# Performance work log

Measured on AMD Instinct MI355X. Metric: run time of the kernel, lower is better.

Reference implementation:

```python
import jax, jax.numpy as jnp
import numpy as np

V, D, H, L, B, T = 32000, 1024, 16, 4, 2, 2048
DH = D // H
F = 4 * D
EPS = 1e-5


def setup_inputs() -> dict:
    key = jax.random.key(0)
    ks = jax.random.split(key, 16)
    s = 0.02
    n = lambda k, shape: (jax.random.normal(k, shape, jnp.float32) * s)
    inp = {
        "idx": jax.random.randint(ks[0], (B, T), 0, V, dtype=jnp.int64),
        "tok_emb": n(ks[1], (V, D)),
        "pos_emb": n(ks[2], (1, T, D)),
        # per-layer stacked params; Linear weights stored as (in, out)
        "Wq": n(ks[3], (L, D, D)), "bq": jnp.zeros((L, D)),
        "Wk": n(ks[4], (L, D, D)), "bk": jnp.zeros((L, D)),
        "Wv": n(ks[5], (L, D, D)), "bv": jnp.zeros((L, D)),
        "Wo": n(ks[6], (L, D, D)), "bo": jnp.zeros((L, D)),
        "ln1_g": jnp.ones((L, D)), "ln1_b": jnp.zeros((L, D)),
        "W1": n(ks[7], (L, D, F)), "b1": jnp.zeros((L, F)),
        "W2": n(ks[8], (L, F, D)), "b2": jnp.zeros((L, D)),
        "ln2_g": jnp.ones((L, D)), "ln2_b": jnp.zeros((L, D)),
        "lnf_g": jnp.ones((D,)), "lnf_b": jnp.zeros((D,)),
        "lm_W": n(ks[9], (D, V)),
    }
    return inp


def _ln(x, g, b):
    m = jnp.mean(x, axis=-1, keepdims=True)
    v = jnp.mean(jnp.square(x - m), axis=-1, keepdims=True)
    return (x - m) * jax.lax.rsqrt(v + EPS) * g + b


def _band_attn(x, Wq, bq, Wk, bk, Wv, bv, Wo, bo):
    # width-3 causal band: query t attends to keys {t, t-1, t-2}
    b_, t_, _ = x.shape
    q = (x @ Wq + bq).reshape(b_, t_, H, DH)
    k = (x @ Wk + bk).reshape(b_, t_, H, DH)
    v = (x @ Wv + bv).reshape(b_, t_, H, DH)

    def shift(a, o):  # align key at position t-o with query t
        return jnp.pad(a, ((0, 0), (o, 0), (0, 0), (0, 0)))[:, :t_]

    ks_ = jnp.stack([shift(k, o) for o in range(3)], axis=-2)  # (B,T,H,3,DH)
    vs_ = jnp.stack([shift(v, o) for o in range(3)], axis=-2)
    scale = 1.0 / np.sqrt(DH)
    scores = jnp.einsum('bthd,bthod->btho', q, ks_) * scale       # (B,T,H,3)
    pos = jnp.arange(t_)[None, :, None, None]
    off = jnp.arange(3)[None, None, None, :]
    scores = jnp.where(pos >= off, scores, -jnp.inf)
    p = jax.nn.softmax(scores, axis=-1)
    y = jnp.einsum('btho,bthod->bthd', p, vs_).reshape(b_, t_, D)
    return y @ Wo + bo


def reference(idx, tok_emb, pos_emb, Wq, bq, Wk, bk, Wv, bv, Wo, bo,
              ln1_g, ln1_b, W1, b1, W2, b2, ln2_g, ln2_b, lnf_g, lnf_b, lm_W):
    t_ = idx.shape[1]
    x = tok_emb[idx] + pos_emb[:, :t_, :]
    for i in range(L):
        h = _ln(x, ln1_g[i], ln1_b[i])
        x = x + _band_attn(h, Wq[i], bq[i], Wk[i], bk[i], Wv[i], bv[i], Wo[i], bo[i])
        h = _ln(x, ln2_g[i], ln2_b[i])
        h = jax.nn.gelu(h @ W1[i] + b1[i], approximate=False) @ W2[i] + b2[i]
        x = x + h
    x = _ln(x, lnf_g, lnf_b)
    logits = x @ lm_W
    return logits
```

## Files before the change

### kernel.cpp

```cpp
#include <hip/hip_runtime.h>
#include <cstdint>
#include <cstddef>

#define MROWS   4096
#define TSEQ    2048
#define DMODEL  1024
#define NHEAD   16
#define FFN     4096
#define NVOCAB  32000
#define NLAYER  4

typedef float  f32x4  __attribute__((ext_vector_type(4)));
typedef __bf16 bf16x8 __attribute__((ext_vector_type(8)));

#define VMCNT(n) asm volatile("s_waitcnt vmcnt(" #n ")" ::: "memory")
#define LGKM0()  asm volatile("s_waitcnt lgkmcnt(0)" ::: "memory")

__device__ __forceinline__ unsigned short f2bf(float f) {
    unsigned u = __builtin_bit_cast(unsigned, f);
    u += 0x7fffu + ((u >> 16) & 1u);
    return (unsigned short)(u >> 16);
}
__device__ __forceinline__ float bf2f(unsigned short u) {
    return __builtin_bit_cast(float, (unsigned)u << 16);
}

__device__ __forceinline__ float gelu_exact(float v) {
    return 0.5f * v * (1.0f + erff(v * 0.7071067811865476f));
}

__global__ __launch_bounds__(256) void embed_kernel(const int* __restrict__ idx,
                                                    const float* __restrict__ tok,
                                                    const float* __restrict__ pos,
                                                    float* __restrict__ x) {
    int row = blockIdx.x, tid = threadIdx.x;
    int token = idx[row];
    int t = row & (TSEQ - 1);
    float4 a = ((const float4*)(tok + (size_t)token * DMODEL))[tid];
    float4 p = ((const float4*)(pos + (size_t)t * DMODEL))[tid];
    a.x += p.x; a.y += p.y; a.z += p.z; a.w += p.w;
    ((float4*)(x + (size_t)row * DMODEL))[tid] = a;
}

__global__ __launch_bounds__(256) void ln_kernel(const float* __restrict__ x,
                                                 const float* __restrict__ g,
                                                 const float* __restrict__ b,
                                                 unsigned short* __restrict__ out) {
    int row = blockIdx.x, tid = threadIdx.x;
    float4 v = ((const float4*)(x + (size_t)row * DMODEL))[tid];
    float s1 = v.x + v.y + v.z + v.w;
    float s2 = v.x * v.x + v.y * v.y + v.z * v.z + v.w * v.w;
    for (int s = 32; s; s >>= 1) { s1 += __shfl_xor(s1, s); s2 += __shfl_xor(s2, s); }
    __shared__ float red[8];
    int lane = tid & 63, w = tid >> 6;
    if (lane == 0) { red[w] = s1; red[4 + w] = s2; }
    __syncthreads();
    s1 = red[0] + red[1] + red[2] + red[3];
    s2 = red[4] + red[5] + red[6] + red[7];
    float mean = s1 * (1.0f / DMODEL);
    float var  = s2 * (1.0f / DMODEL) - mean * mean;
    float rs   = rsqrtf(var + 1e-5f);
    float4 gv = ((const float4*)g)[tid];
    float4 bv = ((const float4*)b)[tid];
    size_t o = (size_t)row * DMODEL + tid * 4;
    out[o + 0] = f2bf((v.x - mean) * rs * gv.x + bv.x);
    out[o + 1] = f2bf((v.y - mean) * rs * gv.y + bv.y);
    out[o + 2] = f2bf((v.z - mean) * rs * gv.z + bv.z);
    out[o + 3] = f2bf((v.w - mean) * rs * gv.w + bv.w);
}

__global__ __launch_bounds__(256) void transpose_bf16(const float* __restrict__ W,
                                                      unsigned short* __restrict__ WT,
                                                      int K, int ldW) {
    __shared__ float tile[64][65];
    int n0 = blockIdx.x * 64, k0 = blockIdx.y * 64;
    int tid = threadIdx.x;
    int lr4 = tid & 15;
    int rw  = tid >> 4;
#pragma unroll
    for (int p = 0; p < 4; ++p) {
        int k = rw + p * 16;
        float4 v = *(const float4*)(W + (size_t)(k0 + k) * ldW + n0 + lr4 * 4);
        tile[k][lr4 * 4 + 0] = v.x;
        tile[k][lr4 * 4 + 1] = v.y;
        tile[k][lr4 * 4 + 2] = v.z;
        tile[k][lr4 * 4 + 3] = v.w;
    }
    __syncthreads();
    int kc = tid & 15;
    int nr = tid >> 4;
#pragma unroll
    for (int p = 0; p < 4; ++p) {
        int n = nr + p * 16;
        ushort4 o;
        o.x = f2bf(tile[kc * 4 + 0][n]);
        o.y = f2bf(tile[kc * 4 + 1][n]);
        o.z = f2bf(tile[kc * 4 + 2][n]);
        o.w = f2bf(tile[kc * 4 + 3][n]);
        *(ushort4*)(WT + (size_t)(n0 + n) * K + k0 + kc * 4) = o;
    }
}

__global__ __launch_bounds__(256) void transpose_qkv(const float* __restrict__ Wq,
                                                     const float* __restrict__ Wk,
                                                     const float* __restrict__ Wv,
                                                     unsigned short* __restrict__ WT) {
    __shared__ float tile[64][65];
    const float* W = (blockIdx.z == 0) ? Wq : (blockIdx.z == 1) ? Wk : Wv;
    unsigned short* dst = WT + (size_t)blockIdx.z * DMODEL * DMODEL;
    int n0 = blockIdx.x * 64, k0 = blockIdx.y * 64;
    int tid = threadIdx.x;
    int lr4 = tid & 15, rw = tid >> 4;
#pragma unroll
    for (int p = 0; p < 4; ++p) {
        int k = rw + p * 16;
        float4 v = *(const float4*)(W + (size_t)(k0 + k) * DMODEL + n0 + lr4 * 4);
        tile[k][lr4 * 4 + 0] = v.x;
        tile[k][lr4 * 4 + 1] = v.y;
        tile[k][lr4 * 4 + 2] = v.z;
        tile[k][lr4 * 4 + 3] = v.w;
    }
    __syncthreads();
    int kc = tid & 15, nr = tid >> 4;
#pragma unroll
    for (int p = 0; p < 4; ++p) {
        int n = nr + p * 16;
        ushort4 o;
        o.x = f2bf(tile[kc * 4 + 0][n]);
        o.y = f2bf(tile[kc * 4 + 1][n]);
        o.z = f2bf(tile[kc * 4 + 2][n]);
        o.w = f2bf(tile[kc * 4 + 3][n]);
        *(ushort4*)(dst + (size_t)(n0 + n) * DMODEL + k0 + kc * 4) = o;
    }
}

__global__ __launch_bounds__(256) void pack_qkv_bias(const float* __restrict__ bq,
                                                     const float* __restrict__ bk,
                                                     const float* __restrict__ bv,
                                                     float* __restrict__ dst) {
    int i = blockIdx.x * 256 + threadIdx.x;
    int l = i / 3072, c = i % 3072;
    float v = (c < 1024) ? bq[l * 1024 + c]
            : (c < 2048) ? bk[l * 1024 + c - 1024]
                         : bv[l * 1024 + c - 2048];
    dst[i] = v;
}

__global__ __launch_bounds__(256) void combine2(const float* __restrict__ p0,
                                                const float* __restrict__ p1,
                                                const float* __restrict__ bias,
                                                float* __restrict__ x) {
    int i = blockIdx.x * 256 + threadIdx.x;
    float4 a = ((const float4*)p0)[i];
    float4 b = ((const float4*)p1)[i];
    float4 xv = ((float4*)x)[i];
    int col = (i * 4) & (DMODEL - 1);
    float4 bb = *(const float4*)(bias + col);
    xv.x += a.x + b.x + bb.x;
    xv.y += a.y + b.y + bb.y;
    xv.z += a.z + b.z + bb.z;
    xv.w += a.w + b.w + bb.w;
    ((float4*)x)[i] = xv;
}

__global__ __launch_bounds__(256) void attn_kernel(const unsigned short* __restrict__ qkv,
                                                   unsigned short* __restrict__ y) {
    int wid  = (blockIdx.x * 256 + threadIdx.x) >> 6;
    int lane = threadIdx.x & 63;
    int h = wid & (NHEAD - 1);
    int row = wid >> 4;
    int t = row & (TSEQ - 1);
    const unsigned short* base = qkv + (size_t)row * 3072 + h * 64;
    float qd = bf2f(base[lane]);
    float d0 = qd * bf2f(base[1024 + lane]);
    float d1 = (t >= 1) ? qd * bf2f(base[1024 - 3072 + lane]) : 0.0f;
    float d2 = (t >= 2) ? qd * bf2f(base[1024 - 6144 + lane]) : 0.0f;
    for (int s = 32; s; s >>= 1) {
        d0 += __shfl_xor(d0, s); d1 += __shfl_xor(d1, s); d2 += __shfl_xor(d2, s);
    }
    d0 *= 0.125f; d1 *= 0.125f; d2 *= 0.125f;
    float m = d0;
    if (t >= 1) m = fmaxf(m, d1);
    if (t >= 2) m = fmaxf(m, d2);
    float p0 = expf(d0 - m);
    float p1 = (t >= 1) ? expf(d1 - m) : 0.0f;
    float p2 = (t >= 2) ? expf(d2 - m) : 0.0f;
    float den = p0 + p1 + p2;
    float v0 = bf2f(base[2048 + lane]);
    float v1 = (t >= 1) ? bf2f(base[2048 - 3072 + lane]) : 0.0f;
    float v2 = (t >= 2) ? bf2f(base[2048 - 6144 + lane]) : 0.0f;
    float yv = (p0 * v0 + p1 * v1 + p2 * v2) / den;
    y[(size_t)row * DMODEL + h * 64 + lane] = f2bf(yv);
}

template <int EPI>
__global__ __launch_bounds__(256, 3) void gemmv2(const unsigned short* __restrict__ A,
                                                 const unsigned short* __restrict__ BT,
                                                 const float* __restrict__ bias,
                                                 const float* __restrict__ res,
                                                 float* __restrict__ outF,
                                                 unsigned short* __restrict__ outB,
                                                 int M, int N, int Ks, int KL, int ldc) {
    __shared__ unsigned short As[2][4096];
    __shared__ unsigned short Bs[2][4096];
    const int tid = threadIdx.x;
    const int lane = tid & 63, wid = tid >> 6;
    const int wr = wid >> 1, wc = wid & 1;
    const int lr = lane & 15, kq = lane >> 4;

    const int nbm = M >> 7;
    const int nwg = gridDim.x;
    int orig = blockIdx.x;
    int q8 = nwg >> 3, r8 = nwg & 7;
    int xcd = orig & 7, lin = orig >> 3;
    int wg = (xcd < r8 ? xcd * (q8 + 1) : r8 * (q8 + 1) + (xcd - r8) * q8) + lin;
    int bm = wg % nbm, bn = wg / nbm;
    const int kc = blockIdx.y;

    const unsigned short* Ab = A + (size_t)bm * 128 * Ks + (size_t)kc * KL;
    const unsigned short* Bb = BT + (size_t)bn * 128 * Ks + (size_t)kc * KL;

    int sOff[2];
#pragma unroll
    for (int i = 0; i < 2; ++i) {
        int pc = i * 256 + tid;
        int line = pc >> 3, slot = pc & 7;
        int row = line * 2 + (slot >> 2);
        int c = (slot & 3) ^ (line & 3);
        sOff[i] = row * Ks + c * 8;
    }

#define STAGEV2(T) do {                                                                        \
    unsigned short* dA_ = &As[(T) & 1][0];                                                     \
    unsigned short* dB_ = &Bs[(T) & 1][0];                                                     \
    _Pragma("unroll") for (int i_ = 0; i_ < 2; ++i_) {                                         \
        __builtin_amdgcn_global_load_lds(                                                      \
            (const __attribute__((address_space(1))) void*)(Ab + sOff[i_] + (T) * 32),         \
            (__attribute__((address_space(3))) void*)(dA_ + (size_t)(i_ * 256 + tid) * 8), 16, 0, 0); \
        __builtin_amdgcn_global_load_lds(                                                      \
            (const __attribute__((address_space(1))) void*)(Bb + sOff[i_] + (T) * 32),         \
            (__attribute__((address_space(3))) void*)(dB_ + (size_t)(i_ * 256 + tid) * 8), 16, 0, 0); \
    }                                                                                          \
} while (0)

    const int slot = ((lane & 1) << 2) | (kq ^ ((lr >> 1) & 3));
    const int laneOff = ((lr >> 1) << 6) + slot * 8;
    int aOff[4], bOff[4];
#pragma unroll
    for (int m = 0; m < 4; ++m) aOff[m] = wr * 2048 + m * 512 + laneOff;
#pragma unroll
    for (int n = 0; n < 4; ++n) bOff[n] = wc * 2048 + n * 512 + laneOff;

    f32x4 acc[4][4] = {};
    const int nt = KL >> 5;

    STAGEV2(0);
    __syncthreads();

    for (int t = 0; t < nt; ++t) {
        const bool pf = (t + 1) < nt;
        if (pf) STAGEV2(t + 1);
        const unsigned short* sA = &As[t & 1][0];
        const unsigned short* sB = &Bs[t & 1][0];
        bf16x8 a[4], b[4];
#pragma unroll
        for (int m = 0; m < 4; ++m) a[m] = *(const bf16x8*)(sA + aOff[m]);
#pragma unroll
        for (int n = 0; n < 4; ++n) b[n] = *(const bf16x8*)(sB + bOff[n]);
        __builtin_amdgcn_s_setprio(1);
#pragma unroll
        for (int m = 0; m < 4; ++m)
#pragma unroll
            for (int n = 0; n < 4; ++n)
                acc[m][n] = __builtin_amdgcn_mfma_f32_16x16x32_bf16(a[m], b[n], acc[m][n], 0, 0, 0);
        __builtin_amdgcn_s_setprio(0);
        if (pf) __syncthreads();
    }

    const int row0 = bm * 128 + wr * 64;
    const int col0 = bn * 128 + wc * 64;
    float* outP = (EPI == 0) ? (outF + (size_t)kc * M * ldc) : outF;
#pragma unroll
    for (int m = 0; m < 4; ++m) {
#pragma unroll
        for (int n = 0; n < 4; ++n) {
            int col = col0 + n * 16 + lr;
            int rbase = row0 + m * 16 + kq * 4;
            float bb = (EPI != 0 && bias) ? bias[col] : 0.0f;
#pragma unroll
            for (int j = 0; j < 4; ++j) {
                size_t off = (size_t)(rbase + j) * ldc + col;
                float v = acc[m][n][j] + bb;
                if (EPI == 1) v += res[off];
                if (EPI == 2)      outB[off] = f2bf(gelu_exact(v));
                else               outP[off] = v;
            }
        }
    }
#undef STAGEV2
}

template <int EPI>
__global__ __launch_bounds__(512, 2) void gemm256(const unsigned short* __restrict__ A,
                                                  const unsigned short* __restrict__ BT,
                                                  const float* __restrict__ bias,
                                                  const float* __restrict__ res,
                                                  float* __restrict__ outF,
                                                  unsigned short* __restrict__ outB,
                                                  int M, int N, int K, int ldc) {
    __shared__ unsigned short As[2][2][8192];
    __shared__ unsigned short Bs[2][2][8192];
    const int tid = threadIdx.x;
    const int lane = tid & 63, wid = tid >> 6;
    const int wr = wid >> 2, wc = wid & 3;
    const int lr = lane & 15, kq = lane >> 4;

    const int nbm = M >> 8;
    const int nwg = gridDim.x;
    int orig = blockIdx.x;
    int q8 = nwg >> 3, r8 = nwg & 7;
    int xcd = orig & 7, lin = orig >> 3;
    int wg = (xcd < r8 ? xcd * (q8 + 1) : r8 * (q8 + 1) + (xcd - r8) * q8) + lin;
    int bm = wg % nbm, bn = wg / nbm;

    const unsigned short* Ab = A + (size_t)bm * 256 * K;
    const unsigned short* Bb = BT + (size_t)bn * 256 * K;

    int sG0, sG1;
    {
        int pc0 = tid,        l0 = pc0 >> 3, s0 = pc0 & 7;
        int pc1 = 512 + tid,  l1 = pc1 >> 3, s1 = pc1 & 7;
        sG0 = (l0 * 2 + (s0 >> 2)) * K + (((s0 & 3) ^ (l0 & 3)) * 8);
        sG1 = (l1 * 2 + (s1 >> 2)) * K + (((s1 & 3) ^ (l1 & 3)) * 8);
    }

#define STAGE256(REGION, GBASE, TT, KH) do {                                                   \
    __builtin_amdgcn_global_load_lds(                                                          \
        (const __attribute__((address_space(1))) void*)((GBASE) + sG0 + (TT) * 64 + (KH) * 32),\
        (__attribute__((address_space(3))) void*)((REGION) + (size_t)tid * 8), 16, 0, 0);      \
    __builtin_amdgcn_global_load_lds(                                                          \
        (const __attribute__((address_space(1))) void*)((GBASE) + sG1 + (TT) * 64 + (KH) * 32),\
        (__attribute__((address_space(3))) void*)((REGION) + (size_t)(512 + tid) * 8), 16, 0, 0);\
} while (0)

    const int slot = ((lane & 1) << 2) | (kq ^ ((lr >> 1) & 3));
    const int laneOff = ((lr >> 1) << 6) + slot * 8;
    const int aBase = wr * 4096 + laneOff;
    const int bBase = wc * 2048 + laneOff;

    f32x4 acc[8][4] = {};
    const int nt = K >> 6;

    STAGE256(&As[0][0][0], Ab, 0, 0);
    STAGE256(&Bs[0][0][0], Bb, 0, 0);
    STAGE256(&As[0][1][0], Ab, 0, 1);
    STAGE256(&Bs[0][1][0], Bb, 0, 1);
    VMCNT(4);
    __builtin_amdgcn_s_barrier();

    for (int t = 0; t < nt; ++t) {
        const int buf = t & 1;
        const bool pf = (t + 1) < nt;
        const unsigned short* A0 = &As[buf][0][0];
        const unsigned short* A1 = &As[buf][1][0];
        const unsigned short* B0 = &Bs[buf][0][0];
        const unsigned short* B1 = &Bs[buf][1][0];
        unsigned short* nA0 = &As[buf ^ 1][0][0];
        unsigned short* nA1 = &As[buf ^ 1][1][0];
        unsigned short* nB0 = &Bs[buf ^ 1][0][0];
        unsigned short* nB1 = &Bs[buf ^ 1][1][0];

        bf16x8 a[8], b0, b1;

#pragma unroll
        for (int m = 0; m < 8; ++m) a[m] = *(const bf16x8*)(A0 + aBase + m * 512);
        b0 = *(const bf16x8*)(B0 + bBase + 0 * 512);
        b1 = *(const bf16x8*)(B0 + bBase + 1 * 512);
        if (pf) STAGE256(nA0, Ab, t + 1, 0);
        __builtin_amdgcn_s_barrier();
        LGKM0();
        __builtin_amdgcn_s_setprio(1);
#pragma unroll
        for (int m = 0; m < 8; ++m) {
            acc[m][0] = __builtin_amdgcn_mfma_f32_16x16x32_bf16(a[m], b0, acc[m][0], 0, 0, 0);
            acc[m][1] = __builtin_amdgcn_mfma_f32_16x16x32_bf16(a[m], b1, acc[m][1], 0, 0, 0);
        }
        __builtin_amdgcn_s_setprio(0);
        __builtin_amdgcn_s_barrier();

        b0 = *(const bf16x8*)(B0 + bBase + 2 * 512);
        b1 = *(const bf16x8*)(B0 + bBase + 3 * 512);
        if (pf) STAGE256(nB0, Bb, t + 1, 0);
        __builtin_amdgcn_s_barrier();
        LGKM0();
        __builtin_amdgcn_s_setprio(1);
#pragma unroll
        for (int m = 0; m < 8; ++m) {
            acc[m][2] = __builtin_amdgcn_mfma_f32_16x16x32_bf16(a[m], b0, acc[m][2], 0, 0, 0);
            acc[m][3] = __builtin_amdgcn_mfma_f32_16x16x32_bf16(a[m], b1, acc[m][3], 0, 0, 0);
        }
        __builtin_amdgcn_s_setprio(0);
        if (pf) VMCNT(4); else VMCNT(0);
        __builtin_amdgcn_s_barrier();

#pragma unroll
        for (int m = 0; m < 8; ++m) a[m] = *(const bf16x8*)(A1 + aBase + m * 512);
        b0 = *(const bf16x8*)(B1 + bBase + 0 * 512);
        b1 = *(const bf16x8*)(B1 + bBase + 1 * 512);
        if (pf) STAGE256(nA1, Ab, t + 1, 1);
        __builtin_amdgcn_s_barrier();
        LGKM0();
        __builtin_amdgcn_s_setprio(1);
#pragma unroll
        for (int m = 0; m < 8; ++m) {
            acc[m][0] = __builtin_amdgcn_mfma_f32_16x16x32_bf16(a[m], b0, acc[m][0], 0, 0, 0);
            acc[m][1] = __builtin_amdgcn_mfma_f32_16x16x32_bf16(a[m], b1, acc[m][1], 0, 0, 0);
        }
        __builtin_amdgcn_s_setprio(0);
        __builtin_amdgcn_s_barrier();

        b0 = *(const bf16x8*)(B1 + bBase + 2 * 512);
        b1 = *(const bf16x8*)(B1 + bBase + 3 * 512);
        if (pf) STAGE256(nB1, Bb, t + 1, 1);
        __builtin_amdgcn_s_barrier();
        LGKM0();
        __builtin_amdgcn_s_setprio(1);
#pragma unroll
        for (int m = 0; m < 8; ++m) {
            acc[m][2] = __builtin_amdgcn_mfma_f32_16x16x32_bf16(a[m], b0, acc[m][2], 0, 0, 0);
            acc[m][3] = __builtin_amdgcn_mfma_f32_16x16x32_bf16(a[m], b1, acc[m][3], 0, 0, 0);
        }
        __builtin_amdgcn_s_setprio(0);
        if (pf) VMCNT(4);
        __builtin_amdgcn_s_barrier();
    }

    const int row0 = bm * 256 + wr * 128;
    const int col0 = bn * 256 + wc * 64;
#pragma unroll
    for (int m = 0; m < 8; ++m) {
#pragma unroll
        for (int n = 0; n < 4; ++n) {
            int col = col0 + n * 16 + lr;
            int rbase = row0 + m * 16 + kq * 4;
            float bb = bias ? bias[col] : 0.0f;
#pragma unroll
            for (int j = 0; j < 4; ++j) {
                size_t off = (size_t)(rbase + j) * ldc + col;
                float v = acc[m][n][j] + bb;
                if (EPI == 1) v += res[off];
                if (EPI == 2)      outB[off] = f2bf(gelu_exact(v));
                else if (EPI == 3) outB[off] = f2bf(v);
                else               outF[off] = v;
            }
        }
    }
#undef STAGE256
}

extern "C" void kernel_launch(void* const* d_in, const int* in_sizes, int n_in,
                              void* d_out, int out_size, void* d_ws, size_t ws_size,
                              hipStream_t stream) {
    const int*   idx  = (const int*)d_in[0];
    const float* tok  = (const float*)d_in[1];
    const float* pos  = (const float*)d_in[2];
    const float* Wq   = (const float*)d_in[3];
    const float* bq   = (const float*)d_in[4];
    const float* Wk   = (const float*)d_in[5];
    const float* bk   = (const float*)d_in[6];
    const float* Wv   = (const float*)d_in[7];
    const float* bv   = (const float*)d_in[8];
    const float* Wo   = (const float*)d_in[9];
    const float* bo   = (const float*)d_in[10];
    const float* ln1g = (const float*)d_in[11];
    const float* ln1b = (const float*)d_in[12];
    const float* W1   = (const float*)d_in[13];
    const float* b1   = (const float*)d_in[14];
    const float* W2   = (const float*)d_in[15];
    const float* b2   = (const float*)d_in[16];
    const float* ln2g = (const float*)d_in[17];
    const float* ln2b = (const float*)d_in[18];
    const float* lnfg = (const float*)d_in[19];
    const float* lnfb = (const float*)d_in[20];
    const float* lmW  = (const float*)d_in[21];

    const bool bigws = ws_size >= (92ull << 20);

    char* ws = (char*)d_ws;
    unsigned short* wbuf;
    unsigned short* hbuf;
    unsigned short* ybuf;
    unsigned short* xfbuf;
    float*          bqkv;
    if (bigws) {
        wbuf  = (unsigned short*)(ws);
        hbuf  = (unsigned short*)(ws + (63ull << 20));
        ybuf  = (unsigned short*)(ws + (71ull << 20));
        xfbuf = (unsigned short*)(ws + (79ull << 20));
        bqkv  = (float*)(ws + (87ull << 20));
    } else {
        wbuf  = (unsigned short*)(ws);
        hbuf  = (unsigned short*)(ws + (16u << 20));
        ybuf  = (unsigned short*)(ws + (24u << 20));
        xfbuf = (unsigned short*)(ws + (32u << 20));
        bqkv  = (float*)(ws + (40u << 20));
    }

    float* outF = (float*)d_out;
    float* xbuf = outF;
    unsigned short* qkv = (unsigned short*)((char*)d_out + (16ull << 20));
    unsigned short* hidden = (unsigned short*)((char*)d_out + (64ull << 20));
    float* pbuf = (float*)((char*)d_out + (96ull << 20));

    embed_kernel<<<MROWS, 256, 0, stream>>>(idx, tok, pos, xbuf);
    pack_qkv_bias<<<(NLAYER * 3072) / 256, 256, 0, stream>>>(bq, bk, bv, bqkv);

    for (int l = 0; l < NLAYER; l++) {
        const size_t wl = (size_t)l * DMODEL * DMODEL;
        ln_kernel<<<MROWS, 256, 0, stream>>>(xbuf, ln1g + l * DMODEL, ln1b + l * DMODEL, hbuf);

        transpose_qkv<<<dim3(16, 16, 3), 256, 0, stream>>>(Wq + wl, Wk + wl, Wv + wl, wbuf);
        gemm256<3><<<dim3((3072 / 256) * (MROWS / 256)), 512, 0, stream>>>(
            hbuf, wbuf, bqkv + l * 3072, nullptr, nullptr, qkv, MROWS, 3072, DMODEL, 3072);

        attn_kernel<<<MROWS * NHEAD / 4, 256, 0, stream>>>(qkv, ybuf);

        transpose_bf16<<<dim3(16, 16), 256, 0, stream>>>(Wo + wl, wbuf, DMODEL, DMODEL);
        gemmv2<1><<<dim3((MROWS / 128) * (DMODEL / 128), 1), 256, 0, stream>>>(
            ybuf, wbuf, bo + l * DMODEL, xbuf, xbuf, nullptr, MROWS, DMODEL, DMODEL, DMODEL, DMODEL);

        ln_kernel<<<MROWS, 256, 0, stream>>>(xbuf, ln2g + l * DMODEL, ln2b + l * DMODEL, hbuf);

        transpose_bf16<<<dim3(FFN / 64, DMODEL / 64), 256, 0, stream>>>(W1 + (size_t)l * DMODEL * FFN, wbuf, DMODEL, FFN);
        gemmv2<2><<<dim3((MROWS / 128) * (FFN / 128), 1), 256, 0, stream>>>(
            hbuf, wbuf, b1 + l * FFN, nullptr, nullptr, hidden, MROWS, FFN, DMODEL, DMODEL, FFN);

        transpose_bf16<<<dim3(DMODEL / 64, FFN / 64), 256, 0, stream>>>(W2 + (size_t)l * FFN * DMODEL, wbuf, FFN, DMODEL);
        gemmv2<0><<<dim3((MROWS / 128) * (DMODEL / 128), 2), 256, 0, stream>>>(
            hidden, wbuf, nullptr, nullptr, pbuf, nullptr, MROWS, DMODEL, FFN, FFN / 2, DMODEL);
        combine2<<<MROWS * DMODEL / 4 / 256, 256, 0, stream>>>(
            pbuf, pbuf + (size_t)MROWS * DMODEL, b2 + l * DMODEL, xbuf);
    }

    ln_kernel<<<MROWS, 256, 0, stream>>>(xbuf, lnfg, lnfb, xfbuf);

    if (bigws) {
        transpose_bf16<<<dim3(NVOCAB / 64, DMODEL / 64), 256, 0, stream>>>(lmW, wbuf, DMODEL, NVOCAB);
        gemm256<0><<<dim3((NVOCAB / 256) * (MROWS / 256)), 512, 0, stream>>>(
            xfbuf, wbuf, nullptr, nullptr, outF, nullptr, MROWS, NVOCAB, DMODEL, NVOCAB);
    } else {
        const int NCHUNK = 6400;
        for (int c = 0; c < NVOCAB / NCHUNK; c++) {
            int n0 = c * NCHUNK;
            transpose_bf16<<<dim3(NCHUNK / 64, DMODEL / 64), 256, 0, stream>>>(lmW + n0, wbuf, DMODEL, NVOCAB);
            gemm256<0><<<dim3((NCHUNK / 256) * (MROWS / 256)), 512, 0, stream>>>(
                xfbuf, wbuf, nullptr, nullptr, outF + n0, nullptr, MROWS, NCHUNK, DMODEL, NVOCAB);
        }
    }
}
```

Baseline: 1.322 ms.

## Simplify 256-tile GEMM to single-stage K=32 double buffer; use 128-tile GEMM for QKV

The 256x256 GEMM's hand-interleaved pipeline (K=64 tiles split into halves, with many barriers and explicit waitcnts) is replaced by a simpler loop. Each iteration stages one K=32 tile into a double buffer and does a full 8x4 MFMA block, with LDS halved and a launch bound of 4 waves per SIMD. The QKV projection moves back to the 128-tile gemmv2 kernel with a new bf16 epilogue, and the 256 kernel now only serves the LM head. The cost is coarser overlap: there is one __syncthreads per K=32 step, and it relies on the compiler to insert waits for the async LDS loads.

```diff
diff --git a/kernel.cpp b/kernel.cpp
--- a/kernel.cpp
+++ b/kernel.cpp
@@ -12,9 +12,6 @@
 
 typedef float  f32x4  __attribute__((ext_vector_type(4)));
 typedef __bf16 bf16x8 __attribute__((ext_vector_type(8)));
-
-#define VMCNT(n) asm volatile("s_waitcnt vmcnt(" #n ")" ::: "memory")
-#define LGKM0()  asm volatile("s_waitcnt lgkmcnt(0)" ::: "memory")
 
 __device__ __forceinline__ unsigned short f2bf(float f) {
     unsigned u = __builtin_bit_cast(unsigned, f);
@@ -293,6 +290,7 @@
                 float v = acc[m][n][j] + bb;
                 if (EPI == 1) v += res[off];
                 if (EPI == 2)      outB[off] = f2bf(gelu_exact(v));
+                else if (EPI == 3) outB[off] = f2bf(v);
                 else               outP[off] = v;
             }
         }
@@ -300,16 +298,12 @@
 #undef STAGEV2
 }
 
-template <int EPI>
-__global__ __launch_bounds__(512, 2) void gemm256(const unsigned short* __restrict__ A,
-                                                  const unsigned short* __restrict__ BT,
-                                                  const float* __restrict__ bias,
-                                                  const float* __restrict__ res,
-                                                  float* __restrict__ outF,
-                                                  unsigned short* __restrict__ outB,
-                                                  int M, int N, int K, int ldc) {
-    __shared__ unsigned short As[2][2][8192];
-    __shared__ unsigned short Bs[2][2][8192];
+__global__ __launch_bounds__(512, 4) void gemm256v3(const unsigned short* __restrict__ A,
+                                                    const unsigned short* __restrict__ BT,
+                                                    float* __restrict__ outF,
+                                                    int M, int N, int K, int ldc) {
+    __shared__ unsigned short As[2][8192];
+    __shared__ unsigned short Bs[2][8192];
     const int tid = threadIdx.x;
     const int lane = tid & 63, wid = tid >> 6;
     const int wr = wid >> 2, wc = wid & 3;
@@ -326,113 +320,61 @@
     const unsigned short* Ab = A + (size_t)bm * 256 * K;
     const unsigned short* Bb = BT + (size_t)bn * 256 * K;
 
-    int sG0, sG1;
-    {
-        int pc0 = tid,        l0 = pc0 >> 3, s0 = pc0 & 7;
-        int pc1 = 512 + tid,  l1 = pc1 >> 3, s1 = pc1 & 7;
-        sG0 = (l0 * 2 + (s0 >> 2)) * K + (((s0 & 3) ^ (l0 & 3)) * 8);
-        sG1 = (l1 * 2 + (s1 >> 2)) * K + (((s1 & 3) ^ (l1 & 3)) * 8);
-    }
-
-#define STAGE256(REGION, GBASE, TT, KH) do {                                                   \
-    __builtin_amdgcn_global_load_lds(                                                          \
-        (const __attribute__((address_space(1))) void*)((GBASE) + sG0 + (TT) * 64 + (KH) * 32),\
-        (__attribute__((address_space(3))) void*)((REGION) + (size_t)tid * 8), 16, 0, 0);      \
-    __builtin_amdgcn_global_load_lds(                                                          \
-        (const __attribute__((address_space(1))) void*)((GBASE) + sG1 + (TT) * 64 + (KH) * 32),\
-        (__attribute__((address_space(3))) void*)((REGION) + (size_t)(512 + tid) * 8), 16, 0, 0);\
+    int sOff[2];
+#pragma unroll
+    for (int i = 0; i < 2; ++i) {
+        int pc = i * 512 + tid;
+        int line = pc >> 3, slot = pc & 7;
+        int row = line * 2 + (slot >> 2);
+        int c = (slot & 3) ^ (line & 3);
+        sOff[i] = row * K + c * 8;
+    }
+
+#define STAGEV3(T) do {                                                                        \
+    unsigned short* dA_ = &As[(T) & 1][0];                                                     \
+    unsigned short* dB_ = &Bs[(T) & 1][0];                                                     \
+    _Pragma("unroll") for (int i_ = 0; i_ < 2; ++i_) {                                         \
+        __builtin_amdgcn_global_load_lds(                                                      \
+            (const __attribute__((address_space(1))) void*)(Ab + sOff[i_] + (T) * 32),         \
+            (__attribute__((address_space(3))) void*)(dA_ + (size_t)(i_ * 512 + tid) * 8), 16, 0, 0); \
+        __builtin_amdgcn_global_load_lds(                                                      \
+            (const __attribute__((address_space(1))) void*)(Bb + sOff[i_] + (T) * 32),         \
+            (__attribute__((address_space(3))) void*)(dB_ + (size_t)(i_ * 512 + tid) * 8), 16, 0, 0); \
+    }                                                                                          \
 } while (0)
 
     const int slot = ((lane & 1) << 2) | (kq ^ ((lr >> 1) & 3));
     const int laneOff = ((lr >> 1) << 6) + slot * 8;
-    const int aBase = wr * 4096 + laneOff;
-    const int bBase = wc * 2048 + laneOff;
+    int aOff[8], bOff[4];
+#pragma unroll
+    for (int m = 0; m < 8; ++m) aOff[m] = wr * 4096 + m * 512 + laneOff;
+#pragma unroll
+    for (int n = 0; n < 4; ++n) bOff[n] = wc * 2048 + n * 512 + laneOff;
 
     f32x4 acc[8][4] = {};
-    const int nt = K >> 6;
-
-    STAGE256(&As[0][0][0], Ab, 0, 0);
-    STAGE256(&Bs[0][0][0], Bb, 0, 0);
-    STAGE256(&As[0][1][0], Ab, 0, 1);
-    STAGE256(&Bs[0][1][0], Bb, 0, 1);
-    VMCNT(4);
-    __builtin_amdgcn_s_barrier();
+    const int nt = K >> 5;
+
+    STAGEV3(0);
+    __syncthreads();
 
     for (int t = 0; t < nt; ++t) {
-        const int buf = t & 1;
         const bool pf = (t + 1) < nt;
-        const unsigned short* A0 = &As[buf][0][0];
-        const unsigned short* A1 = &As[buf][1][0];
-        const unsigned short* B0 = &Bs[buf][0][0];
-        const unsigned short* B1 = &Bs[buf][1][0];
-        unsigned short* nA0 = &As[buf ^ 1][0][0];
-        unsigned short* nA1 = &As[buf ^ 1][1][0];
-        unsigned short* nB0 = &Bs[buf ^ 1][0][0];
-        unsigned short* nB1 = &Bs[buf ^ 1][1][0];
-
-        bf16x8 a[8], b0, b1;
-
-#pragma unroll
-        for (int m = 0; m < 8; ++m) a[m] = *(const bf16x8*)(A0 + aBase + m * 512);
-        b0 = *(const bf16x8*)(B0 + bBase + 0 * 512);
-        b1 = *(const bf16x8*)(B0 + bBase + 1 * 512);
-        if (pf) STAGE256(nA0, Ab, t + 1, 0);
-        __builtin_amdgcn_s_barrier();
-        LGKM0();
+        if (pf) STAGEV3(t + 1);
+        const unsigned short* sA = &As[t & 1][0];
+        const unsigned short* sB = &Bs[t & 1][0];
+        bf16x8 a[8], b[4];
+#pragma unroll
+        for (int m = 0; m < 8; ++m) a[m] = *(const bf16x8*)(sA + aOff[m]);
+#pragma unroll
+        for (int n = 0; n < 4; ++n) b[n] = *(const bf16x8*)(sB + bOff[n]);
         __builtin_amdgcn_s_setprio(1);
 #pragma unroll
-        for (int m = 0; m < 8; ++m) {
-            acc[m][0] = __builtin_amdgcn_mfma_f32_16x16x32_bf16(a[m], b0, acc[m][0], 0, 0, 0);
-            acc[m][1] = __builtin_amdgcn_mfma_f32_16x16x32_bf16(a[m], b1, acc[m][1], 0, 0, 0);
-        }
+        for (int m = 0; m < 8; ++m)
+#pragma unroll
+            for (int n = 0; n < 4; ++n)
+                acc[m][n] = __builtin_amdgcn_mfma_f32_16x16x32_bf16(a[m], b[n], acc[m][n], 0, 0, 0);
         __builtin_amdgcn_s_setprio(0);
-        __builtin_amdgcn_s_barrier();
-
-        b0 = *(const bf16x8*)(B0 + bBase + 2 * 512);
-        b1 = *(const bf16x8*)(B0 + bBase + 3 * 512);
-        if (pf) STAGE256(nB0, Bb, t + 1, 0);
-        __builtin_amdgcn_s_barrier();
-        LGKM0();
-        __builtin_amdgcn_s_setprio(1);
-#pragma unroll
-        for (int m = 0; m < 8; ++m) {
-            acc[m][2] = __builtin_amdgcn_mfma_f32_16x16x32_bf16(a[m], b0, acc[m][2], 0, 0, 0);
-            acc[m][3] = __builtin_amdgcn_mfma_f32_16x16x32_bf16(a[m], b1, acc[m][3], 0, 0, 0);
-        }
-        __builtin_amdgcn_s_setprio(0);
-        if (pf) VMCNT(4); else VMCNT(0);
-        __builtin_amdgcn_s_barrier();
-
-#pragma unroll
-        for (int m = 0; m < 8; ++m) a[m] = *(const bf16x8*)(A1 + aBase + m * 512);
-        b0 = *(const bf16x8*)(B1 + bBase + 0 * 512);
-        b1 = *(const bf16x8*)(B1 + bBase + 1 * 512);
-        if (pf) STAGE256(nA1, Ab, t + 1, 1);
-        __builtin_amdgcn_s_barrier();
-        LGKM0();
-        __builtin_amdgcn_s_setprio(1);
-#pragma unroll
-        for (int m = 0; m < 8; ++m) {
-            acc[m][0] = __builtin_amdgcn_mfma_f32_16x16x32_bf16(a[m], b0, acc[m][0], 0, 0, 0);
-            acc[m][1] = __builtin_amdgcn_mfma_f32_16x16x32_bf16(a[m], b1, acc[m][1], 0, 0, 0);
-        }
-        __builtin_amdgcn_s_setprio(0);
-        __builtin_amdgcn_s_barrier();
-
-        b0 = *(const bf16x8*)(B1 + bBase + 2 * 512);
-        b1 = *(const bf16x8*)(B1 + bBase + 3 * 512);
-        if (pf) STAGE256(nB1, Bb, t + 1, 1);
-        __builtin_amdgcn_s_barrier();
-        LGKM0();
-        __builtin_amdgcn_s_setprio(1);
-#pragma unroll
-        for (int m = 0; m < 8; ++m) {
-            acc[m][2] = __builtin_amdgcn_mfma_f32_16x16x32_bf16(a[m], b0, acc[m][2], 0, 0, 0);
-            acc[m][3] = __builtin_amdgcn_mfma_f32_16x16x32_bf16(a[m], b1, acc[m][3], 0, 0, 0);
-        }
-        __builtin_amdgcn_s_setprio(0);
-        if (pf) VMCNT(4);
-        __builtin_amdgcn_s_barrier();
+        if (pf) __syncthreads();
     }
 
     const int row0 = bm * 256 + wr * 128;
@@ -443,19 +385,14 @@
         for (int n = 0; n < 4; ++n) {
             int col = col0 + n * 16 + lr;
             int rbase = row0 + m * 16 + kq * 4;
-            float bb = bias ? bias[col] : 0.0f;
 #pragma unroll
             for (int j = 0; j < 4; ++j) {
                 size_t off = (size_t)(rbase + j) * ldc + col;
-                float v = acc[m][n][j] + bb;
-                if (EPI == 1) v += res[off];
-                if (EPI == 2)      outB[off] = f2bf(gelu_exact(v));
-                else if (EPI == 3) outB[off] = f2bf(v);
-                else               outF[off] = v;
+                outF[off] = acc[m][n][j];
             }
         }
     }
-#undef STAGE256
+#undef STAGEV3
 }
 
 extern "C" void kernel_launch(void* const* d_in, const int* in_sizes, int n_in,
@@ -520,8 +457,8 @@
         ln_kernel<<<MROWS, 256, 0, stream>>>(xbuf, ln1g + l * DMODEL, ln1b + l * DMODEL, hbuf);
 
         transpose_qkv<<<dim3(16, 16, 3), 256, 0, stream>>>(Wq + wl, Wk + wl, Wv + wl, wbuf);
-        gemm256<3><<<dim3((3072 / 256) * (MROWS / 256)), 512, 0, stream>>>(
-            hbuf, wbuf, bqkv + l * 3072, nullptr, nullptr, qkv, MROWS, 3072, DMODEL, 3072);
+        gemmv2<3><<<dim3((MROWS / 128) * (3072 / 128), 1), 256, 0, stream>>>(
+            hbuf, wbuf, bqkv + l * 3072, nullptr, nullptr, qkv, MROWS, 3072, DMODEL, DMODEL, 3072);
 
         attn_kernel<<<MROWS * NHEAD / 4, 256, 0, stream>>>(qkv, ybuf);
 
@@ -546,15 +483,15 @@
 
     if (bigws) {
         transpose_bf16<<<dim3(NVOCAB / 64, DMODEL / 64), 256, 0, stream>>>(lmW, wbuf, DMODEL, NVOCAB);
-        gemm256<0><<<dim3((NVOCAB / 256) * (MROWS / 256)), 512, 0, stream>>>(
-            xfbuf, wbuf, nullptr, nullptr, outF, nullptr, MROWS, NVOCAB, DMODEL, NVOCAB);
+        gemm256v3<<<dim3((NVOCAB / 256) * (MROWS / 256)), 512, 0, stream>>>(
+            xfbuf, wbuf, outF, MROWS, NVOCAB, DMODEL, NVOCAB);
     } else {
         const int NCHUNK = 6400;
         for (int c = 0; c < NVOCAB / NCHUNK; c++) {
             int n0 = c * NCHUNK;
             transpose_bf16<<<dim3(NCHUNK / 64, DMODEL / 64), 256, 0, stream>>>(lmW + n0, wbuf, DMODEL, NVOCAB);
-            gemm256<0><<<dim3((NCHUNK / 256) * (MROWS / 256)), 512, 0, stream>>>(
-                xfbuf, wbuf, nullptr, nullptr, outF + n0, nullptr, MROWS, NCHUNK, DMODEL, NVOCAB);
+            gemm256v3<<<dim3((NCHUNK / 256) * (MROWS / 256)), 512, 0, stream>>>(
+                xfbuf, wbuf, outF + n0, MROWS, NCHUNK, DMODEL, NVOCAB);
         }
     }
 }
```

Result: slower. 3.557 ms (+169.1%).

## Restructure 256-tile GEMM pipeline into two half-K phases; route QKV to 128 GEMM

Applied to the files above, without the earlier changes.

The 256x256 GEMM main loop is reorganised so each 32-wide K half loads all A and B fragments at once, issues both A and B prefetches together, and runs a full 8x4 MFMA block. This halves the barriers per iteration and turns it into a specialised logits-only kernel with a plain fp32 store. The QKV projection moves to the 128-tile gemmv2 kernel with a new bf16-store epilogue, giving more workgroups for that smaller GEMM. The trade-off is higher register pressure from holding all fragments and less interleaving between LDS reads and MFMA work.

```diff
diff --git a/kernel.cpp b/kernel.cpp
--- a/kernel.cpp
+++ b/kernel.cpp
@@ -293,6 +293,7 @@
                 float v = acc[m][n][j] + bb;
                 if (EPI == 1) v += res[off];
                 if (EPI == 2)      outB[off] = f2bf(gelu_exact(v));
+                else if (EPI == 3) outB[off] = f2bf(v);
                 else               outP[off] = v;
             }
         }
@@ -300,14 +301,10 @@
 #undef STAGEV2
 }
 
-template <int EPI>
-__global__ __launch_bounds__(512, 2) void gemm256(const unsigned short* __restrict__ A,
-                                                  const unsigned short* __restrict__ BT,
-                                                  const float* __restrict__ bias,
-                                                  const float* __restrict__ res,
-                                                  float* __restrict__ outF,
-                                                  unsigned short* __restrict__ outB,
-                                                  int M, int N, int K, int ldc) {
+__global__ __launch_bounds__(512, 2) void gemm256lp(const unsigned short* __restrict__ A,
+                                                    const unsigned short* __restrict__ BT,
+                                                    float* __restrict__ outF,
+                                                    int M, int N, int K, int ldc) {
     __shared__ unsigned short As[2][2][8192];
     __shared__ unsigned short Bs[2][2][8192];
     const int tid = threadIdx.x;
@@ -355,84 +352,58 @@
     STAGE256(&Bs[0][0][0], Bb, 0, 0);
     STAGE256(&As[0][1][0], Ab, 0, 1);
     STAGE256(&Bs[0][1][0], Bb, 0, 1);
-    VMCNT(4);
-    __builtin_amdgcn_s_barrier();
 
     for (int t = 0; t < nt; ++t) {
         const int buf = t & 1;
         const bool pf = (t + 1) < nt;
-        const unsigned short* A0 = &As[buf][0][0];
-        const unsigned short* A1 = &As[buf][1][0];
-        const unsigned short* B0 = &Bs[buf][0][0];
-        const unsigned short* B1 = &Bs[buf][1][0];
-        unsigned short* nA0 = &As[buf ^ 1][0][0];
-        unsigned short* nA1 = &As[buf ^ 1][1][0];
-        unsigned short* nB0 = &Bs[buf ^ 1][0][0];
-        unsigned short* nB1 = &Bs[buf ^ 1][1][0];
-
-        bf16x8 a[8], b0, b1;
-
-#pragma unroll
-        for (int m = 0; m < 8; ++m) a[m] = *(const bf16x8*)(A0 + aBase + m * 512);
-        b0 = *(const bf16x8*)(B0 + bBase + 0 * 512);
-        b1 = *(const bf16x8*)(B0 + bBase + 1 * 512);
-        if (pf) STAGE256(nA0, Ab, t + 1, 0);
+
+        VMCNT(4);
         __builtin_amdgcn_s_barrier();
-        LGKM0();
-        __builtin_amdgcn_s_setprio(1);
-#pragma unroll
-        for (int m = 0; m < 8; ++m) {
-            acc[m][0] = __builtin_amdgcn_mfma_f32_16x16x32_bf16(a[m], b0, acc[m][0], 0, 0, 0);
-            acc[m][1] = __builtin_amdgcn_mfma_f32_16x16x32_bf16(a[m], b1, acc[m][1], 0, 0, 0);
+        {
+            const unsigned short* A0 = &As[buf][0][0];
+            const unsigned short* B0 = &Bs[buf][0][0];
+            bf16x8 a[8], b[4];
+#pragma unroll
+            for (int m = 0; m < 8; ++m) a[m] = *(const bf16x8*)(A0 + aBase + m * 512);
+#pragma unroll
+            for (int n = 0; n < 4; ++n) b[n] = *(const bf16x8*)(B0 + bBase + n * 512);
+            if (pf) {
+                STAGE256(&As[buf ^ 1][0][0], Ab, t + 1, 0);
+                STAGE256(&Bs[buf ^ 1][0][0], Bb, t + 1, 0);
+            }
+            LGKM0();
+            __builtin_amdgcn_s_setprio(1);
+#pragma unroll
+            for (int m = 0; m < 8; ++m)
+#pragma unroll
+                for (int n = 0; n < 4; ++n)
+                    acc[m][n] = __builtin_amdgcn_mfma_f32_16x16x32_bf16(a[m], b[n], acc[m][n], 0, 0, 0);
+            __builtin_amdgcn_s_setprio(0);
         }
-        __builtin_amdgcn_s_setprio(0);
-        __builtin_amdgcn_s_barrier();
-
-        b0 = *(const bf16x8*)(B0 + bBase + 2 * 512);
-        b1 = *(const bf16x8*)(B0 + bBase + 3 * 512);
-        if (pf) STAGE256(nB0, Bb, t + 1, 0);
-        __builtin_amdgcn_s_barrier();
-        LGKM0();
-        __builtin_amdgcn_s_setprio(1);
-#pragma unroll
-        for (int m = 0; m < 8; ++m) {
-            acc[m][2] = __builtin_amdgcn_mfma_f32_16x16x32_bf16(a[m], b0, acc[m][2], 0, 0, 0);
-            acc[m][3] = __builtin_amdgcn_mfma_f32_16x16x32_bf16(a[m], b1, acc[m][3], 0, 0, 0);
-        }
-        __builtin_amdgcn_s_setprio(0);
+
         if (pf) VMCNT(4); else VMCNT(0);
         __builtin_amdgcn_s_barrier();
-
-#pragma unroll
-        for (int m = 0; m < 8; ++m) a[m] = *(const bf16x8*)(A1 + aBase + m * 512);
-        b0 = *(const bf16x8*)(B1 + bBase + 0 * 512);
-        b1 = *(const bf16x8*)(B1 + bBase + 1 * 512);
-        if (pf) STAGE256(nA1, Ab, t + 1, 1);
-        __builtin_amdgcn_s_barrier();
-        LGKM0();
-        __builtin_amdgcn_s_setprio(1);
-#pragma unroll
-        for (int m = 0; m < 8; ++m) {
-            acc[m][0] = __builtin_amdgcn_mfma_f32_16x16x32_bf16(a[m], b0, acc[m][0], 0, 0, 0);
-            acc[m][1] = __builtin_amdgcn_mfma_f32_16x16x32_bf16(a[m], b1, acc[m][1], 0, 0, 0);
+        {
+            const unsigned short* A1 = &As[buf][1][0];
+            const unsigned short* B1 = &Bs[buf][1][0];
+            bf16x8 a[8], b[4];
+#pragma unroll
+            for (int m = 0; m < 8; ++m) a[m] = *(const bf16x8*)(A1 + aBase + m * 512);
+#pragma unroll
+            for (int n = 0; n < 4; ++n) b[n] = *(const bf16x8*)(B1 + bBase + n * 512);
+            if (pf) {
+                STAGE256(&As[buf ^ 1][1][0], Ab, t + 1, 1);
+                STAGE256(&Bs[buf ^ 1][1][0], Bb, t + 1, 1);
+            }
+            LGKM0();
+            __builtin_amdgcn_s_setprio(1);
+#pragma unroll
+            for (int m = 0; m < 8; ++m)
+#pragma unroll
+                for (int n = 0; n < 4; ++n)
+                    acc[m][n] = __builtin_amdgcn_mfma_f32_16x16x32_bf16(a[m], b[n], acc[m][n], 0, 0, 0);
+            __builtin_amdgcn_s_setprio(0);
         }
-        __builtin_amdgcn_s_setprio(0);
-        __builtin_amdgcn_s_barrier();
-
-        b0 = *(const bf16x8*)(B1 + bBase + 2 * 512);
-        b1 = *(const bf16x8*)(B1 + bBase + 3 * 512);
-        if (pf) STAGE256(nB1, Bb, t + 1, 1);
-        __builtin_amdgcn_s_barrier();
-        LGKM0();
-        __builtin_amdgcn_s_setprio(1);
-#pragma unroll
-        for (int m = 0; m < 8; ++m) {
-            acc[m][2] = __builtin_amdgcn_mfma_f32_16x16x32_bf16(a[m], b0, acc[m][2], 0, 0, 0);
-            acc[m][3] = __builtin_amdgcn_mfma_f32_16x16x32_bf16(a[m], b1, acc[m][3], 0, 0, 0);
-        }
-        __builtin_amdgcn_s_setprio(0);
-        if (pf) VMCNT(4);
-        __builtin_amdgcn_s_barrier();
     }
 
     const int row0 = bm * 256 + wr * 128;
@@ -443,15 +414,10 @@
         for (int n = 0; n < 4; ++n) {
             int col = col0 + n * 16 + lr;
             int rbase = row0 + m * 16 + kq * 4;
-            float bb = bias ? bias[col] : 0.0f;
 #pragma unroll
             for (int j = 0; j < 4; ++j) {
                 size_t off = (size_t)(rbase + j) * ldc + col;
-                float v = acc[m][n][j] + bb;
-                if (EPI == 1) v += res[off];
-                if (EPI == 2)      outB[off] = f2bf(gelu_exact(v));
-                else if (EPI == 3) outB[off] = f2bf(v);
-                else               outF[off] = v;
+                outF[off] = acc[m][n][j];
             }
         }
     }
@@ -520,8 +486,8 @@
         ln_kernel<<<MROWS, 256, 0, stream>>>(xbuf, ln1g + l * DMODEL, ln1b + l * DMODEL, hbuf);
 
         transpose_qkv<<<dim3(16, 16, 3), 256, 0, stream>>>(Wq + wl, Wk + wl, Wv + wl, wbuf);
-        gemm256<3><<<dim3((3072 / 256) * (MROWS / 256)), 512, 0, stream>>>(
-            hbuf, wbuf, bqkv + l * 3072, nullptr, nullptr, qkv, MROWS, 3072, DMODEL, 3072);
+        gemmv2<3><<<dim3((MROWS / 128) * (3072 / 128), 1), 256, 0, stream>>>(
+            hbuf, wbuf, bqkv + l * 3072, nullptr, nullptr, qkv, MROWS, 3072, DMODEL, DMODEL, 3072);
 
         attn_kernel<<<MROWS * NHEAD / 4, 256, 0, stream>>>(qkv, ybuf);
 
@@ -546,15 +512,15 @@
 
     if (bigws) {
         transpose_bf16<<<dim3(NVOCAB / 64, DMODEL / 64), 256, 0, stream>>>(lmW, wbuf, DMODEL, NVOCAB);
-        gemm256<0><<<dim3((NVOCAB / 256) * (MROWS / 256)), 512, 0, stream>>>(
-            xfbuf, wbuf, nullptr, nullptr, outF, nullptr, MROWS, NVOCAB, DMODEL, NVOCAB);
+        gemm256lp<<<dim3((NVOCAB / 256) * (MROWS / 256)), 512, 0, stream>>>(
+            xfbuf, wbuf, outF, MROWS, NVOCAB, DMODEL, NVOCAB);
     } else {
         const int NCHUNK = 6400;
         for (int c = 0; c < NVOCAB / NCHUNK; c++) {
             int n0 = c * NCHUNK;
             transpose_bf16<<<dim3(NCHUNK / 64, DMODEL / 64), 256, 0, stream>>>(lmW + n0, wbuf, DMODEL, NVOCAB);
-            gemm256<0><<<dim3((NCHUNK / 256) * (MROWS / 256)), 512, 0, stream>>>(
-                xfbuf, wbuf, nullptr, nullptr, outF + n0, nullptr, MROWS, NCHUNK, DMODEL, NVOCAB);
+            gemm256lp<<<dim3((NCHUNK / 256) * (MROWS / 256)), 512, 0, stream>>>(
+                xfbuf, wbuf, outF + n0, MROWS, NCHUNK, DMODEL, NVOCAB);
         }
     }
 }
```

Result: no change. 1.306 ms (-1.2%).
